# Performance work log

Hardware: AMD Instinct MI355X
Metric: run time of the kernel (lower is better)

## Reference

```python
import jax, jax.numpy as jnp
import numpy as np
import math

B, S, D, H = 2, 1024, 1024, 16
HD = D // H
MAX_ITERS = 4
BETA_0, BETA_DELTA = 0.8, 0.2
MOMENTUM = 0.2
FREQ_FACTOR, PHASE_OFFSET = 2.0, 0.0


def setup_inputs() -> dict:
    key = jax.random.key(0)
    ks = jax.random.split(key, 10)
    s = 1.0 / math.sqrt(D)
    return {
        "x": jax.random.normal(ks[0], (B, S, D), dtype=jnp.float32),
        "Wq": jax.random.normal(ks[1], (D, D), dtype=jnp.float32) * s,
        "bq": jnp.zeros((D,), dtype=jnp.float32),
        "Wk": jax.random.normal(ks[2], (D, D), dtype=jnp.float32) * s,
        "bk": jnp.zeros((D,), dtype=jnp.float32),
        "Wv": jax.random.normal(ks[3], (D, D), dtype=jnp.float32) * s,
        "bv": jnp.zeros((D,), dtype=jnp.float32),
        "Wo": jax.random.normal(ks[4], (D, D), dtype=jnp.float32) * s,
        "bo": jnp.zeros((D,), dtype=jnp.float32),
        "resonance_bias": jnp.zeros((1, H, 1, 1), dtype=jnp.float32),
        "phase_factors": jnp.full((1, H, 1, 1), 0.1, dtype=jnp.float32),
    }


def reference(x, Wq, bq, Wk, bk, Wv, bv, Wo, bo, resonance_bias, phase_factors):
    # Projections -> [B, H, S, HD]
    def split_heads(t):
        return t.reshape(B, S, H, HD).transpose(0, 2, 1, 3)

    q = split_heads(x @ Wq.T + bq)
    k = split_heads(x @ Wk.T + bk)
    v = split_heads(x @ Wv.T + bv)

    scale = 1.0 / math.sqrt(HD)
    attn = None
    for t in range(MAX_ITERS):
        # Phase modulation: shift Q/K by learned per-head phase factors
        t_norm = t / MAX_ITERS
        phase = jnp.sin(jnp.float32(FREQ_FACTOR * t_norm * math.pi + PHASE_OFFSET))
        q_mod = q + phase_factors * phase
        k_mod = k + phase_factors * phase
        # Temperature scheduling: inverse temperature grows each iteration
        beta = BETA_0 + BETA_DELTA * t
        scores = beta * scale * jnp.einsum("bhsd,bhtd->bhst", q_mod, k_mod) + resonance_bias
        attn_new = jax.nn.softmax(scores, axis=-1)
        # Momentum-based attention update
        attn = attn_new if attn is None else MOMENTUM * attn + (1.0 - MOMENTUM) * attn_new

    ctx = jnp.einsum("bhst,bhtd->bhsd", attn, v)  # [B,H,S,HD]
    ctx = ctx.transpose(0, 2, 1, 3).reshape(B, S, D)
    return ctx @ Wo.T + bo
```

## Files before the change

### kernel.cpp

```cpp
#include <hip/hip_runtime.h>
#include <hip/hip_bf16.h>
#include <math.h>

#define BB 2
#define SS 1024
#define DD 1024
#define HH 16
#define HD 64
#define BH (BB*HH)

typedef __attribute__((ext_vector_type(8))) short short8_t;
typedef __attribute__((ext_vector_type(4))) float f32x4;

#if __has_builtin(__builtin_amdgcn_exp2f)
#define EXP2(x) __builtin_amdgcn_exp2f(x)
#else
#define EXP2(x) exp2f(x)
#endif

__device__ __forceinline__ ushort f2bf(float f) {
    union { float f; unsigned u; } a; a.f = f;
    unsigned u = a.u;
    u += 0x7FFFu + ((u >> 16) & 1u);
    return (ushort)(u >> 16);
}
__device__ __forceinline__ float bf2f(ushort b) {
    union { unsigned u; float f; } a; a.u = ((unsigned)b) << 16;
    return a.f;
}
__device__ __forceinline__ unsigned pkbf(float a, float b) {
    unsigned r;
    asm("v_cvt_pk_bf16_f32 %0, %1, %2" : "=v"(r) : "v"(a), "v"(b));
    return r;
}

__global__ __launch_bounds__(256) void cvt_all_kernel(
    const float* __restrict__ x,  const float* __restrict__ wq,
    const float* __restrict__ wk, const float* __restrict__ wv,
    const float* __restrict__ wo,
    ushort* __restrict__ xb,  ushort* __restrict__ wqb, ushort* __restrict__ wkb,
    ushort* __restrict__ wvb, ushort* __restrict__ wob)
{
    int bid = blockIdx.x;
    const float* src; ushort* dst; int off;
    if (bid < 2048) { src = x; dst = xb; off = bid; }
    else {
        int seg = (bid - 2048) >> 10;
        off = (bid - 2048) & 1023;
        if (seg == 0)      { src = wq; dst = wqb; }
        else if (seg == 1) { src = wk; dst = wkb; }
        else if (seg == 2) { src = wv; dst = wvb; }
        else               { src = wo; dst = wob; }
    }
    int i = (off * 256 + threadIdx.x) * 4;
    float4 v = *reinterpret_cast<const float4*>(src + i);
    ushort4 o;
    o.x = f2bf(v.x); o.y = f2bf(v.y); o.z = f2bf(v.z); o.w = f2bf(v.w);
    *reinterpret_cast<ushort4*>(dst + i) = o;
}

template<int BM, int OUT_F32>
__device__ __forceinline__ void gemm_body(
    const ushort* __restrict__ A, const ushort* __restrict__ Bm,
    const float* __restrict__ bias, void* __restrict__ Cout,
    int N, int K, float scale, int omode)
{
    constexpr int BK = 32;
    __shared__ ushort lsa[BM * BK];
    __shared__ ushort lsb[128 * BK];
    const int tid  = threadIdx.x;
    const int lane = tid & 63;
    const int wave = tid >> 6;
    constexpr int RI = BM / 32;
    const int wrow = (wave >> 1) * (BM / 2);
    const int wcol = (wave & 1) * 64;
    const int tileM = blockIdx.y * BM;
    const int tileN = blockIdx.x * 128;
    const int fr  = lane & 15;
    const int fks = (lane >> 4) * 8;
    const int l4  = lane >> 2;
    const int lm4 = lane & 3;
    f32x4 acc[RI][4] = {};

    for (int kb = 0; kb < K; kb += BK) {
        __syncthreads();
        #pragma unroll
        for (int i = 0; i < BM / 64; ++i) {
            int chunk = wave * (BM / 64) + i;
            const ushort* g = A + (size_t)(tileM + chunk * 16 + l4) * K + kb + lm4 * 8;
            __builtin_amdgcn_global_load_lds(
                (const __attribute__((address_space(1))) unsigned*)g,
                (__attribute__((address_space(3))) unsigned*)&lsa[chunk * 512], 16, 0, 0);
        }
        #pragma unroll
        for (int i = 0; i < 2; ++i) {
            int chunk = wave * 2 + i;
            const ushort* g = Bm + (size_t)(tileN + chunk * 16 + l4) * K + kb + lm4 * 8;
            __builtin_amdgcn_global_load_lds(
                (const __attribute__((address_space(1))) unsigned*)g,
                (__attribute__((address_space(3))) unsigned*)&lsb[chunk * 512], 16, 0, 0);
        }
        __syncthreads();
        short8_t af[RI], bfg[4];
        #pragma unroll
        for (int r = 0; r < RI; ++r)
            af[r] = *reinterpret_cast<const short8_t*>(&lsa[(wrow + r * 16 + fr) * BK + fks]);
        #pragma unroll
        for (int c = 0; c < 4; ++c)
            bfg[c] = *reinterpret_cast<const short8_t*>(&lsb[(wcol + c * 16 + fr) * BK + fks]);
        #pragma unroll
        for (int r = 0; r < RI; ++r)
            #pragma unroll
            for (int c = 0; c < 4; ++c)
                acc[r][c] = __builtin_amdgcn_mfma_f32_16x16x32_bf16(af[r], bfg[c], acc[r][c], 0, 0, 0);
    }

    const int rr = (lane >> 4) * 4;
    #pragma unroll
    for (int r = 0; r < RI; ++r) {
        #pragma unroll
        for (int c = 0; c < 4; ++c) {
            int n = tileN + wcol + c * 16 + fr;
            float bv = bias[n];
            #pragma unroll
            for (int q = 0; q < 4; ++q) {
                int m = tileM + wrow + r * 16 + rr + q;
                float v = (acc[r][c][q] + bv) * scale;
                if (OUT_F32) {
                    ((float*)Cout)[(size_t)m * N + n] = v;
                } else if (omode == 0) {
                    ((ushort*)Cout)[(size_t)m * N + n] = f2bf(v);
                } else {
                    int bh = ((m >> 10) << 4) + (n >> 6);
                    int j  = m & 1023;
                    int d  = n & 63;
                    if (omode == 2)
                        ((ushort*)Cout)[((size_t)bh * 1024 + j) * 64 + d] = f2bf(v);
                    else
                        ((ushort*)Cout)[(((size_t)(bh * 32 + (j >> 5)) * 64 + d)) * 32 + (j & 31)] = f2bf(v);
                }
            }
        }
    }
}

__global__ __launch_bounds__(256) void gemm_qkv_kernel(
    const ushort* __restrict__ xb,
    const ushort* __restrict__ wq, const ushort* __restrict__ wk, const ushort* __restrict__ wv,
    const float* __restrict__ bq, const float* __restrict__ bk, const float* __restrict__ bv,
    ushort* __restrict__ Qb, ushort* __restrict__ Kh, ushort* __restrict__ Vt2, float qscale)
{
    const ushort* Bm; const float* bias; ushort* out; float sc; int omode;
    if (blockIdx.z == 0)      { Bm = wq; bias = bq; out = Qb;  sc = qscale; omode = 0; }
    else if (blockIdx.z == 1) { Bm = wk; bias = bk; out = Kh;  sc = 1.0f;   omode = 2; }
    else                      { Bm = wv; bias = bv; out = Vt2; sc = 1.0f;   omode = 3; }
    gemm_body<64, 0>(xb, Bm, bias, out, DD, DD, sc, omode);
}

__global__ __launch_bounds__(256) void gemm_out_kernel(
    const ushort* __restrict__ ctxb, const ushort* __restrict__ wo,
    const float* __restrict__ bo, float* __restrict__ out)
{
    gemm_body<64, 1>(ctxb, wo, bo, out, DD, DD, 1.0f, 0);
}

__global__ __launch_bounds__(256) void tables_kernel(const ushort* __restrict__ Kh,
                                                     const float* __restrict__ pf,
                                                     float* __restrict__ E1, float* __restrict__ E3,
                                                     float a1, float a3) {
    int idx = blockIdx.x * blockDim.x + threadIdx.x;
    int bh = idx >> 10;
    int h = bh & 15;
    const ushort* kr = Kh + (size_t)idx * HD;
    float s = 0.f;
    #pragma unroll
    for (int c = 0; c < HD; c += 8) {
        short8_t v = *reinterpret_cast<const short8_t*>(kr + c);
        #pragma unroll
        for (int e = 0; e < 8; ++e) s += bf2f((ushort)v[e]);
    }
    float ph = pf[h];
    E1[idx] = __expf(a1 * ph * s);
    E3[idx] = __expf(a3 * ph * s);
}

__global__ __launch_bounds__(256) void attn_kernel(
    const ushort* __restrict__ Qb, const ushort* __restrict__ Kh,
    const ushort* __restrict__ Vt2, const float* __restrict__ E1,
    const float* __restrict__ E3, ushort* __restrict__ ctxb)
{
    __shared__ ushort ycache[4][32][264];
    __shared__ float lbuf[4][4][32];
    const int wg  = blockIdx.x;
    const int swz = (wg & 7) * 128 + (wg >> 3);
    const int bh  = swz >> 5;
    const int qb  = (swz & 31) * 32;
    const int b = bh >> 4, h = bh & 15;
    const int wave = threadIdx.x >> 6;
    const int lane = threadIdx.x & 63;
    const int fr = lane & 15;
    const int g  = lane >> 4;
    const int fk = g * 8;

    const float wt[4] = {0.008f, 0.032f, 0.16f, 0.8f};

    const ushort* qbase0 = Qb + (size_t)(b * SS + qb + fr) * DD + h * HD;
    const ushort* qbase1 = Qb + (size_t)(b * SS + qb + 16 + fr) * DD + h * HD;
    const short8_t aq0a = *reinterpret_cast<const short8_t*>(qbase0 + fk);
    const short8_t aq1a = *reinterpret_cast<const short8_t*>(qbase0 + 32 + fk);
    const short8_t aq0b = *reinterpret_cast<const short8_t*>(qbase1 + fk);
    const short8_t aq1b = *reinterpret_cast<const short8_t*>(qbase1 + 32 + fk);

    const float* e1h = E1 + bh * SS;
    const float* e3h = E3 + bh * SS;
    const ushort* khead = Kh + (size_t)bh * SS * HD;
    const ushort* vhead = Vt2 + (size_t)bh * (SS / 32) * HD * 32;

    float lA[4][4] = {}, lB[4][4] = {};
    for (int it = 0; it < 4; ++it) {
        const int k0 = wave * 256 + it * 64;
        #pragma unroll
        for (int n = 0; n < 4; ++n) {
            const ushort* kb = khead + (size_t)(k0 + n * 16 + fr) * HD;
            short8_t bk0 = *reinterpret_cast<const short8_t*>(kb + fk);
            short8_t bk1 = *reinterpret_cast<const short8_t*>(kb + 32 + fk);
            f32x4 za = {0.f, 0.f, 0.f, 0.f};
            f32x4 zb = {0.f, 0.f, 0.f, 0.f};
            za = __builtin_amdgcn_mfma_f32_16x16x32_bf16(aq0a, bk0, za, 0, 0, 0);
            za = __builtin_amdgcn_mfma_f32_16x16x32_bf16(aq1a, bk1, za, 0, 0, 0);
            zb = __builtin_amdgcn_mfma_f32_16x16x32_bf16(aq0b, bk0, zb, 0, 0, 0);
            zb = __builtin_amdgcn_mfma_f32_16x16x32_bf16(aq1b, bk1, zb, 0, 0, 0);
            float e1v = e1h[k0 + n * 16 + fr];
            float e3v = e3h[k0 + n * 16 + fr];
            #pragma unroll
            for (int r = 0; r < 4; ++r) {
                float ya  = EXP2(za[r]);
                float ya2 = ya * ya;
                float ya4 = ya2 * ya2;
                float ya6 = ya4 * ya2;
                lA[0][r] += ya4;
                lA[1][r] += ya4 * ya * e1v;
                lA[2][r] += ya6;
                lA[3][r] += ya6 * ya * e3v;
                ycache[wave][g * 4 + r][it * 64 + n * 16 + fr] = f2bf(ya);
                float yb  = EXP2(zb[r]);
                float yb2 = yb * yb;
                float yb4 = yb2 * yb2;
                float yb6 = yb4 * yb2;
                lB[0][r] += yb4;
                lB[1][r] += yb4 * yb * e1v;
                lB[2][r] += yb6;
                lB[3][r] += yb6 * yb * e3v;
                ycache[wave][16 + g * 4 + r][it * 64 + n * 16 + fr] = f2bf(yb);
            }
        }
    }
    #pragma unroll
    for (int t = 0; t < 4; ++t)
        #pragma unroll
        for (int r = 0; r < 4; ++r) {
            float sa = lA[t][r];
            sa += __shfl_xor(sa, 1);
            sa += __shfl_xor(sa, 2);
            sa += __shfl_xor(sa, 4);
            sa += __shfl_xor(sa, 8);
            lA[t][r] = sa;
            float sb = lB[t][r];
            sb += __shfl_xor(sb, 1);
            sb += __shfl_xor(sb, 2);
            sb += __shfl_xor(sb, 4);
            sb += __shfl_xor(sb, 8);
            lB[t][r] = sb;
        }
    if (fr == 0) {
        #pragma unroll
        for (int t = 0; t < 4; ++t)
            #pragma unroll
            for (int r = 0; r < 4; ++r) {
                lbuf[wave][t][g * 4 + r]      = lA[t][r];
                lbuf[wave][t][16 + g * 4 + r] = lB[t][r];
            }
    }
    __syncthreads();

    float wlA[4], wlB[4];
    #pragma unroll
    for (int t = 0; t < 4; ++t) {
        float sa = lbuf[0][t][fr] + lbuf[1][t][fr] + lbuf[2][t][fr] + lbuf[3][t][fr];
        float sb = lbuf[0][t][16 + fr] + lbuf[1][t][16 + fr] + lbuf[2][t][16 + fr] + lbuf[3][t][16 + fr];
        wlA[t] = wt[t] / sa;
        wlB[t] = wt[t] / sb;
    }

    f32x4 caccA[4] = {}, caccB[4] = {};
    union FragU { short8_t s; unsigned u[4]; };
    for (int it = 0; it < 4; ++it) {
        const int k0 = wave * 256 + it * 64;
        #pragma unroll
        for (int half = 0; half < 2; ++half) {
            short8_t ya8 = *reinterpret_cast<const short8_t*>(
                &ycache[wave][fr][it * 64 + half * 32 + fk]);
            short8_t yb8 = *reinterpret_cast<const short8_t*>(
                &ycache[wave][16 + fr][it * 64 + half * 32 + fk]);
            const float* e1p = e1h + k0 + half * 32 + fk;
            const float* e3p = e3h + k0 + half * 32 + fk;
            float4 e1a = *reinterpret_cast<const float4*>(e1p);
            float4 e1b = *reinterpret_cast<const float4*>(e1p + 4);
            float4 e3a = *reinterpret_cast<const float4*>(e3p);
            float4 e3b = *reinterpret_cast<const float4*>(e3p + 4);
            FragU paA, paB;
            #pragma unroll
            for (int i = 0; i < 4; ++i) {
                float pva[2], pvb[2];
                #pragma unroll
                for (int j = 0; j < 2; ++j) {
                    const int e = 2 * i + j;
                    float e1v = (e < 4) ? ((const float*)&e1a)[e] : ((const float*)&e1b)[e - 4];
                    float e3v = (e < 4) ? ((const float*)&e3a)[e] : ((const float*)&e3b)[e - 4];
                    float ya  = bf2f((ushort)ya8[e]);
                    float ya2 = ya * ya;
                    float ya4 = ya2 * ya2;
                    float t1a = fmaf(ya, wlA[1] * e1v, wlA[0]);
                    float t2a = fmaf(ya, wlA[3] * e3v, wlA[2]);
                    pva[j] = ya4 * fmaf(ya2, t2a, t1a);
                    float yb  = bf2f((ushort)yb8[e]);
                    float yb2 = yb * yb;
                    float yb4 = yb2 * yb2;
                    float t1b = fmaf(yb, wlB[1] * e1v, wlB[0]);
                    float t2b = fmaf(yb, wlB[3] * e3v, wlB[2]);
                    pvb[j] = yb4 * fmaf(yb2, t2b, t1b);
                }
                paA.u[i] = pkbf(pva[0], pva[1]);
                paB.u[i] = pkbf(pvb[0], pvb[1]);
            }
            const ushort* vt = vhead + (size_t)((k0 + half * 32) >> 5) * HD * 32;
            #pragma unroll
            for (int n2 = 0; n2 < 4; ++n2) {
                short8_t v = *reinterpret_cast<const short8_t*>(
                    vt + (n2 * 16 + fr) * 32 + fk);
                caccA[n2] = __builtin_amdgcn_mfma_f32_16x16x32_bf16(paA.s, v, caccA[n2], 0, 0, 0);
                caccB[n2] = __builtin_amdgcn_mfma_f32_16x16x32_bf16(paB.s, v, caccB[n2], 0, 0, 0);
            }
        }
    }

    __syncthreads();
    float* ctxp = (float*)&ycache[wave][0][0];
    #pragma unroll
    for (int n2 = 0; n2 < 4; ++n2)
        #pragma unroll
        for (int q = 0; q < 4; ++q) {
            ctxp[(g * 4 + q) * 68 + n2 * 16 + fr]        = caccA[n2][q];
            ctxp[(16 + g * 4 + q) * 68 + n2 * 16 + fr]   = caccB[n2][q];
        }
    __syncthreads();

    const int d0 = (threadIdx.x & 15) * 4;
    float* base = (float*)&ycache[0][0][0];
    #pragma unroll
    for (int rr = 0; rr < 2; ++rr) {
        int row = rr * 16 + (threadIdx.x >> 4);
        float4 s0 = *reinterpret_cast<float4*>(base + 0 * 4224 + row * 68 + d0);
        float4 s1 = *reinterpret_cast<float4*>(base + 1 * 4224 + row * 68 + d0);
        float4 s2 = *reinterpret_cast<float4*>(base + 2 * 4224 + row * 68 + d0);
        float4 s3 = *reinterpret_cast<float4*>(base + 3 * 4224 + row * 68 + d0);
        float ox = s0.x + s1.x + s2.x + s3.x;
        float oy = s0.y + s1.y + s2.y + s3.y;
        float oz = s0.z + s1.z + s2.z + s3.z;
        float ow = s0.w + s1.w + s2.w + s3.w;
        uint2 o;
        o.x = pkbf(ox, oy);
        o.y = pkbf(oz, ow);
        size_t off = (size_t)(b * SS + qb + row) * DD + h * HD + d0;
        *reinterpret_cast<uint2*>(ctxb + off) = o;
    }
}

extern "C" void kernel_launch(void* const* d_in, const int* in_sizes, int n_in,
                              void* d_out, int out_size, void* d_ws, size_t ws_size,
                              hipStream_t stream) {
    const float* x  = (const float*)d_in[0];
    const float* Wq = (const float*)d_in[1];
    const float* bq = (const float*)d_in[2];
    const float* Wk = (const float*)d_in[3];
    const float* bk = (const float*)d_in[4];
    const float* Wv = (const float*)d_in[5];
    const float* bv = (const float*)d_in[6];
    const float* Wo = (const float*)d_in[7];
    const float* bo = (const float*)d_in[8];
    const float* pf = (const float*)d_in[10];

    ushort* xb   = (ushort*)d_ws;
    ushort* wqb  = xb  + (size_t)2 * 1024 * 1024;
    ushort* wkb  = wqb + (size_t)1024 * 1024;
    ushort* wvb  = wkb + (size_t)1024 * 1024;
    ushort* wob  = wvb + (size_t)1024 * 1024;
    ushort* Qb   = wob + (size_t)1024 * 1024;
    ushort* Kh   = Qb  + (size_t)2 * 1024 * 1024;
    ushort* Vt2  = Kh  + (size_t)2 * 1024 * 1024;
    ushort* ctxb = Vt2 + (size_t)2 * 1024 * 1024;
    float*  E1p  = (float*)(ctxb + (size_t)2 * 1024 * 1024);
    float*  E3p  = E1p + (size_t)BH * SS;

    float ph[4], ctv[4];
    for (int t = 0; t < 4; ++t) {
        double tn = (double)t / 4.0;
        ph[t]  = sinf((float)(2.0 * tn * M_PI + 0.0));
        ctv[t] = (float)((0.8 + 0.2 * (double)t) * 0.125);
    }
    const double LOG2E = 1.44269504088896340736;
    float qscale = (float)(0.025 * LOG2E);
    float a1 = ctv[1] * ph[1];
    float a3 = ctv[3] * ph[3];

    cvt_all_kernel<<<6144, 256, 0, stream>>>(x, Wq, Wk, Wv, Wo, xb, wqb, wkb, wvb, wob);

    gemm_qkv_kernel<<<dim3(8, 32, 3), 256, 0, stream>>>(xb, wqb, wkb, wvb, bq, bk, bv,
                                                        Qb, Kh, Vt2, qscale);

    tables_kernel<<<BH * SS / 256, 256, 0, stream>>>(Kh, pf, E1p, E3p, a1, a3);

    attn_kernel<<<1024, 256, 0, stream>>>(Qb, Kh, Vt2, E1p, E3p, ctxb);

    gemm_out_kernel<<<dim3(8, 32), 256, 0, stream>>>(ctxb, wob, bo, (float*)d_out);
}
```

Baseline: 105.0 us.

## Fuse K row-sum exp tables into QKV GEMM epilogue and retile output GEMM

Computes the per-row K sums and their E1/E3 exponential tables inside the K-projection GEMM epilogue, using wave shuffles over the accumulators, and removes the separate tables kernel launch and its re-read of K. It also generalises the GEMM body over the N tile size and runs the output projection with 64-wide N tiles on a 16x32 grid to get more workgroups. The fused sums come from fp32 accumulators rather than bf16-rounded K, so the tables differ slightly in value. The smaller output tiles reuse less data per workgroup.

```diff
diff --git a/kernel.cpp b/kernel.cpp
--- a/kernel.cpp
+++ b/kernel.cpp
@@ -59,59 +59,64 @@
     *reinterpret_cast<ushort4*>(dst + i) = o;
 }
 
-template<int BM, int OUT_F32>
+template<int BM, int BN, int OUT_F32>
 __device__ __forceinline__ void gemm_body(
     const ushort* __restrict__ A, const ushort* __restrict__ Bm,
     const float* __restrict__ bias, void* __restrict__ Cout,
-    int N, int K, float scale, int omode)
+    int N, int K, float scale, int omode,
+    const float* __restrict__ pf, float* __restrict__ E1, float* __restrict__ E3,
+    float a1, float a3)
 {
     constexpr int BK = 32;
     __shared__ ushort lsa[BM * BK];
-    __shared__ ushort lsb[128 * BK];
+    __shared__ ushort lsb[BN * BK];
     const int tid  = threadIdx.x;
     const int lane = tid & 63;
     const int wave = tid >> 6;
     constexpr int RI = BM / 32;
+    constexpr int CI = BN / 32;
+    constexpr int ACH = BM / 16;
+    constexpr int TCH = ACH + BN / 16;
     const int wrow = (wave >> 1) * (BM / 2);
-    const int wcol = (wave & 1) * 64;
+    const int wcol = (wave & 1) * (BN / 2);
     const int tileM = blockIdx.y * BM;
-    const int tileN = blockIdx.x * 128;
+    const int tileN = blockIdx.x * BN;
     const int fr  = lane & 15;
     const int fks = (lane >> 4) * 8;
     const int l4  = lane >> 2;
     const int lm4 = lane & 3;
-    f32x4 acc[RI][4] = {};
+    f32x4 acc[RI][CI] = {};
 
     for (int kb = 0; kb < K; kb += BK) {
         __syncthreads();
         #pragma unroll
-        for (int i = 0; i < BM / 64; ++i) {
-            int chunk = wave * (BM / 64) + i;
-            const ushort* g = A + (size_t)(tileM + chunk * 16 + l4) * K + kb + lm4 * 8;
-            __builtin_amdgcn_global_load_lds(
-                (const __attribute__((address_space(1))) unsigned*)g,
-                (__attribute__((address_space(3))) unsigned*)&lsa[chunk * 512], 16, 0, 0);
-        }
-        #pragma unroll
-        for (int i = 0; i < 2; ++i) {
-            int chunk = wave * 2 + i;
-            const ushort* g = Bm + (size_t)(tileN + chunk * 16 + l4) * K + kb + lm4 * 8;
-            __builtin_amdgcn_global_load_lds(
-                (const __attribute__((address_space(1))) unsigned*)g,
-                (__attribute__((address_space(3))) unsigned*)&lsb[chunk * 512], 16, 0, 0);
+        for (int i = 0; i < TCH / 4; ++i) {
+            int chunk = wave * (TCH / 4) + i;
+            if (chunk < ACH) {
+                const ushort* g = A + (size_t)(tileM + chunk * 16 + l4) * K + kb + lm4 * 8;
+                __builtin_amdgcn_global_load_lds(
+                    (const __attribute__((address_space(1))) unsigned*)g,
+                    (__attribute__((address_space(3))) unsigned*)&lsa[chunk * 512], 16, 0, 0);
+            } else {
+                int bc = chunk - ACH;
+                const ushort* g = Bm + (size_t)(tileN + bc * 16 + l4) * K + kb + lm4 * 8;
+                __builtin_amdgcn_global_load_lds(
+                    (const __attribute__((address_space(1))) unsigned*)g,
+                    (__attribute__((address_space(3))) unsigned*)&lsb[bc * 512], 16, 0, 0);
+            }
         }
         __syncthreads();
-        short8_t af[RI], bfg[4];
+        short8_t af[RI], bfg[CI];
         #pragma unroll
         for (int r = 0; r < RI; ++r)
             af[r] = *reinterpret_cast<const short8_t*>(&lsa[(wrow + r * 16 + fr) * BK + fks]);
         #pragma unroll
-        for (int c = 0; c < 4; ++c)
+        for (int c = 0; c < CI; ++c)
             bfg[c] = *reinterpret_cast<const short8_t*>(&lsb[(wcol + c * 16 + fr) * BK + fks]);
         #pragma unroll
         for (int r = 0; r < RI; ++r)
             #pragma unroll
-            for (int c = 0; c < 4; ++c)
+            for (int c = 0; c < CI; ++c)
                 acc[r][c] = __builtin_amdgcn_mfma_f32_16x16x32_bf16(af[r], bfg[c], acc[r][c], 0, 0, 0);
     }
 
@@ -119,7 +124,7 @@
     #pragma unroll
     for (int r = 0; r < RI; ++r) {
         #pragma unroll
-        for (int c = 0; c < 4; ++c) {
+        for (int c = 0; c < CI; ++c) {
             int n = tileN + wcol + c * 16 + fr;
             float bv = bias[n];
             #pragma unroll
@@ -142,46 +147,54 @@
             }
         }
     }
+
+    if (!OUT_F32 && omode == 2 && CI == 4) {
+        int h = ((tileN + wcol) >> 6) & 15;
+        float apf1 = a1 * pf[h];
+        float apf3 = a3 * pf[h];
+        #pragma unroll
+        for (int r = 0; r < RI; ++r) {
+            #pragma unroll
+            for (int q = 0; q < 4; ++q) {
+                float s = 0.f;
+                #pragma unroll
+                for (int c = 0; c < CI; ++c)
+                    s += acc[r][c][q] + bias[tileN + wcol + c * 16 + fr];
+                s += __shfl_xor(s, 1);
+                s += __shfl_xor(s, 2);
+                s += __shfl_xor(s, 4);
+                s += __shfl_xor(s, 8);
+                if (fr == 0) {
+                    int m = tileM + wrow + r * 16 + rr + q;
+                    int idx = ((m >> 10) * 16 + h) * 1024 + (m & 1023);
+                    E1[idx] = __expf(apf1 * s);
+                    E3[idx] = __expf(apf3 * s);
+                }
+            }
+        }
+    }
 }
 
 __global__ __launch_bounds__(256) void gemm_qkv_kernel(
     const ushort* __restrict__ xb,
     const ushort* __restrict__ wq, const ushort* __restrict__ wk, const ushort* __restrict__ wv,
     const float* __restrict__ bq, const float* __restrict__ bk, const float* __restrict__ bv,
-    ushort* __restrict__ Qb, ushort* __restrict__ Kh, ushort* __restrict__ Vt2, float qscale)
+    ushort* __restrict__ Qb, ushort* __restrict__ Kh, ushort* __restrict__ Vt2,
+    const float* __restrict__ pf, float* __restrict__ E1, float* __restrict__ E3,
+    float qscale, float a1, float a3)
 {
     const ushort* Bm; const float* bias; ushort* out; float sc; int omode;
     if (blockIdx.z == 0)      { Bm = wq; bias = bq; out = Qb;  sc = qscale; omode = 0; }
     else if (blockIdx.z == 1) { Bm = wk; bias = bk; out = Kh;  sc = 1.0f;   omode = 2; }
     else                      { Bm = wv; bias = bv; out = Vt2; sc = 1.0f;   omode = 3; }
-    gemm_body<64, 0>(xb, Bm, bias, out, DD, DD, sc, omode);
+    gemm_body<64, 128, 0>(xb, Bm, bias, out, DD, DD, sc, omode, pf, E1, E3, a1, a3);
 }
 
 __global__ __launch_bounds__(256) void gemm_out_kernel(
     const ushort* __restrict__ ctxb, const ushort* __restrict__ wo,
     const float* __restrict__ bo, float* __restrict__ out)
 {
-    gemm_body<64, 1>(ctxb, wo, bo, out, DD, DD, 1.0f, 0);
-}
-
-__global__ __launch_bounds__(256) void tables_kernel(const ushort* __restrict__ Kh,
-                                                     const float* __restrict__ pf,
-                                                     float* __restrict__ E1, float* __restrict__ E3,
-                                                     float a1, float a3) {
-    int idx = blockIdx.x * blockDim.x + threadIdx.x;
-    int bh = idx >> 10;
-    int h = bh & 15;
-    const ushort* kr = Kh + (size_t)idx * HD;
-    float s = 0.f;
-    #pragma unroll
-    for (int c = 0; c < HD; c += 8) {
-        short8_t v = *reinterpret_cast<const short8_t*>(kr + c);
-        #pragma unroll
-        for (int e = 0; e < 8; ++e) s += bf2f((ushort)v[e]);
-    }
-    float ph = pf[h];
-    E1[idx] = __expf(a1 * ph * s);
-    E3[idx] = __expf(a3 * ph * s);
+    gemm_body<64, 64, 1>(ctxb, wo, bo, out, DD, DD, 1.0f, 0, nullptr, nullptr, nullptr, 0.f, 0.f);
 }
 
 __global__ __launch_bounds__(256) void attn_kernel(
@@ -416,11 +429,10 @@
     cvt_all_kernel<<<6144, 256, 0, stream>>>(x, Wq, Wk, Wv, Wo, xb, wqb, wkb, wvb, wob);
 
     gemm_qkv_kernel<<<dim3(8, 32, 3), 256, 0, stream>>>(xb, wqb, wkb, wvb, bq, bk, bv,
-                                                        Qb, Kh, Vt2, qscale);
-
-    tables_kernel<<<BH * SS / 256, 256, 0, stream>>>(Kh, pf, E1p, E3p, a1, a3);
+                                                        Qb, Kh, Vt2, pf, E1p, E3p,
+                                                        qscale, a1, a3);
 
     attn_kernel<<<1024, 256, 0, stream>>>(Qb, Kh, Vt2, E1p, E3p, ctxb);
 
-    gemm_out_kernel<<<dim3(8, 32), 256, 0, stream>>>(ctxb, wob, bo, (float*)d_out);
-}
+    gemm_out_kernel<<<dim3(16, 32), 256, 0, stream>>>(ctxb, wob, bo, (float*)d_out);
+}
```

Result: faster. 99.28 us (-5.4%).
